# Optimization experiments

Measured on AMD Instinct MI355X. Metric: run time of the kernel, lower is better.

The kernel has to match this reference:

```python
import jax, jax.numpy as jnp
import numpy as np

B, K = 4096, 64
D_MODEL, D_DYN, D_STAT = 256, 512, 64
H = 4
DH = D_MODEL // H
SCALE = DH ** -0.5
LN_EPS = 1e-5


def _ln(x, g, b):
    m = x.mean(-1, keepdims=True)
    v = ((x - m) ** 2).mean(-1, keepdims=True)
    return (x - m) * jax.lax.rsqrt(v + LN_EPS) * g + b


def setup_inputs() -> dict:
    key = jax.random.key(0)
    ks = jax.random.split(key, 16)
    w = lambda k, s: jax.random.normal(k, s, jnp.float32) * 0.02
    return {
        "h_dyn": jax.random.normal(ks[0], (B, D_DYN), jnp.float32),
        "x_stat": jax.random.normal(ks[1], (B, K, D_STAT), jnp.float32),
        "W_dyn": w(ks[2], (D_DYN, D_MODEL)), "b_dyn": jnp.zeros((D_MODEL,)),
        "W_stat": w(ks[3], (D_STAT, D_MODEL)), "b_stat": jnp.zeros((D_MODEL,)),
        "g_ndyn": jnp.ones((D_MODEL,)), "b_ndyn": jnp.zeros((D_MODEL,)),
        "g_nstat": jnp.ones((D_MODEL,)), "b_nstat": jnp.zeros((D_MODEL,)),
        "Wq": w(ks[4], (D_MODEL, D_MODEL)), "bq": jnp.zeros((D_MODEL,)),
        "Wk": w(ks[5], (D_MODEL, D_MODEL)), "bk": jnp.zeros((D_MODEL,)),
        "Wv": w(ks[6], (D_MODEL, D_MODEL)), "bv": jnp.zeros((D_MODEL,)),
        "g_mlp": jnp.ones((D_MODEL,)), "b_mlp": jnpp if False else jnp.zeros((D_MODEL,)),
        "W1": w(ks[7], (D_MODEL, D_MODEL)), "b1": jnp.zeros((D_MODEL,)),
        "W2": w(ks[8], (D_MODEL, D_MODEL)), "b2": jnp.zeros((D_MODEL,)),
        "Wo": w(ks[9], (D_MODEL, D_MODEL)), "bo": jnp.zeros((D_MODEL,)),
        "res_scale": jnp.float32(0.1),
    }


def reference(h_dyn, x_stat, W_dyn, b_dyn, W_stat, b_stat, g_ndyn, b_ndyn,
              g_nstat, b_nstat, Wq, bq, Wk, bk, Wv, bv, g_mlp, b_mlp,
              W1, b1, W2, b2, Wo, bo, res_scale):
    h0 = h_dyn @ W_dyn + b_dyn                  # [B, d_model]
    s = x_stat @ W_stat + b_stat                # [B, K, d_model]
    h = _ln(h0, g_ndyn, b_ndyn)
    s = _ln(s, g_nstat, b_nstat)

    q = (h @ Wq + bq).reshape(B, H, DH)         # [B, H, dh]
    k = (s @ Wk + bk).reshape(B, K, H, DH)      # [B, K, H, dh]
    v_flat = s @ Wv + bv                        # [B, K, d_model]

    # per-variable MLP (DeepSets style): LN -> Linear -> GELU(exact) -> Linear
    t = _ln(v_flat, g_mlp, b_mlp)
    t = jax.nn.gelu(t @ W1 + b1, approximate=False)
    v_tokens = t @ W2 + b2                      # [B, K, d_model]

    logits = jnp.einsum('bhd,bkhd->bhk', q, k) * SCALE   # [B, H, K]
    w = jax.nn.sigmoid(logits)
    w = w / (w.sum(-1, keepdims=True) + 1e-6)

    vh = v_tokens.reshape(B, K, H, DH)
    z = jnp.einsum('bhk,bkhd->bhd', w, vh).reshape(B, D_MODEL)
    c = z @ Wo + bo
    c = h0 + res_scale * c
    w_mean = w.mean(axis=1)                     # [B, K]
    return c, w_mean
```

## Files before the change

kernel.cpp:

```cpp
#include <hip/hip_runtime.h>
#include <cmath>


typedef __bf16 bf16;
typedef bf16 bf16x4 __attribute__((ext_vector_type(4)));
typedef bf16 bf16x8 __attribute__((ext_vector_type(8)));
typedef float f32x4 __attribute__((ext_vector_type(4)));

#define MFMA_B16(a, b, c) __builtin_amdgcn_mfma_f32_16x16x32_bf16((a), (b), (c), 0, 0, 0)
#define RCP(x) __builtin_amdgcn_rcpf(x)
#define RSQ(x) __builtin_amdgcn_rsqf(x)

constexpr int SROW = 264;
constexpr int XROW = 72;

constexpr size_t WSTAT_P = 0;
constexpr size_t WV_P    = 16384;
constexpr size_t W1_P    = 81920;
constexpr size_t W2O_P   = 147456;
constexpr size_t WDYN_P  = 212992;
constexpr size_t WQ_P    = 344064;
constexpr size_t WK_P    = 409600;
constexpr size_t KQ_BF   = 475136;
constexpr size_t H0_F   = 2334720;
constexpr size_t BKQ_F  = 3383296;
constexpr size_t B2O_F  = 3399680;
constexpr size_t W2OS_F = 3399936;

__device__ __forceinline__ bf16x8 zero8() {
  bf16x8 z;
#pragma unroll
  for (int j = 0; j < 8; ++j) z[j] = (bf16)0.0f;
  return z;
}

__device__ __forceinline__ float wave_sum(float v) {
#pragma unroll
  for (int m = 1; m < 64; m <<= 1) v += __shfl_xor(v, m, 64);
  return v;
}

__device__ __forceinline__ void zero_acc(f32x4 (&acc)[4][4]) {
#pragma unroll
  for (int mt = 0; mt < 4; ++mt)
#pragma unroll
    for (int nt = 0; nt < 4; ++nt) { f32x4 z = {0.f, 0.f, 0.f, 0.f}; acc[mt][nt] = z; }
}

__device__ __forceinline__ void gemm_swapped_p(const bf16* buf, const bf16* __restrict__ Wp,
                                               int w, int lane, int l16, int koff,
                                               f32x4 (&acc)[4][4]) {
  const bf16* base = Wp + (size_t)w * 8 * 2048 + lane * 8;
  bf16x8 aw[2][4];
#pragma unroll
  for (int dt = 0; dt < 4; ++dt) aw[0][dt] = *(const bf16x8*)(base + dt * 512);
#pragma unroll
  for (int ks = 0; ks < 8; ++ks) {
    const int cur = ks & 1;
    if (ks < 7) {
#pragma unroll
      for (int dt = 0; dt < 4; ++dt)
        aw[cur ^ 1][dt] = *(const bf16x8*)(base + (ks + 1) * 2048 + dt * 512);
    }
#pragma unroll
    for (int tt = 0; tt < 4; ++tt) {
      bf16x8 bfrag = *(const bf16x8*)(buf + (tt * 16 + l16) * SROW + ks * 32 + koff);
#pragma unroll
      for (int dt = 0; dt < 4; ++dt) acc[dt][tt] = MFMA_B16(aw[cur][dt], bfrag, acc[dt][tt]);
    }
  }
}

__device__ __forceinline__ void gemm_orig_p(const bf16* buf, const bf16* __restrict__ Wp,
                                            int w, int lane, int l16, int koff,
                                            f32x4 (&acc)[4][4]) {
  const bf16* base = Wp + (size_t)w * 8 * 2048 + lane * 8;
  bf16x8 bw[2][4];
#pragma unroll
  for (int nt = 0; nt < 4; ++nt) bw[0][nt] = *(const bf16x8*)(base + nt * 512);
#pragma unroll
  for (int ks = 0; ks < 8; ++ks) {
    const int cur = ks & 1;
    if (ks < 7) {
#pragma unroll
      for (int nt = 0; nt < 4; ++nt)
        bw[cur ^ 1][nt] = *(const bf16x8*)(base + (ks + 1) * 2048 + nt * 512);
    }
#pragma unroll
    for (int mt = 0; mt < 4; ++mt) {
      bf16x8 a = *(const bf16x8*)(buf + (mt * 16 + l16) * SROW + ks * 32 + koff);
#pragma unroll
      for (int nt = 0; nt < 4; ++nt) acc[mt][nt] = MFMA_B16(a, bw[cur][nt], acc[mt][nt]);
    }
  }
}

__device__ __forceinline__ void bias_stats(f32x4 (&acc)[4][4], const float* __restrict__ bsrc,
                                           int w, int quad, int l16,
                                           float (*part_s)[64], float (*part_ss)[64]) {
  float ps[4] = {0.f, 0.f, 0.f, 0.f}, pq[4] = {0.f, 0.f, 0.f, 0.f};
#pragma unroll
  for (int dt = 0; dt < 4; ++dt) {
    const float4 bb = *(const float4*)(bsrc + w * 64 + dt * 16 + quad * 4);
#pragma unroll
    for (int tt = 0; tt < 4; ++tt) {
      float v0 = acc[dt][tt][0] + bb.x;
      float v1 = acc[dt][tt][1] + bb.y;
      float v2 = acc[dt][tt][2] + bb.z;
      float v3 = acc[dt][tt][3] + bb.w;
      acc[dt][tt][0] = v0; acc[dt][tt][1] = v1; acc[dt][tt][2] = v2; acc[dt][tt][3] = v3;
      ps[tt] += (v0 + v1) + (v2 + v3);
      pq[tt] += v0 * v0 + v1 * v1 + v2 * v2 + v3 * v3;
    }
  }
#pragma unroll
  for (int tt = 0; tt < 4; ++tt) {
    ps[tt] += __shfl_xor(ps[tt], 16, 64); ps[tt] += __shfl_xor(ps[tt], 32, 64);
    pq[tt] += __shfl_xor(pq[tt], 16, 64); pq[tt] += __shfl_xor(pq[tt], 32, 64);
  }
  if (quad == 0) {
#pragma unroll
    for (int tt = 0; tt < 4; ++tt) {
      part_s[w][tt * 16 + l16] = ps[tt];
      part_ss[w][tt * 16 + l16] = pq[tt];
    }
  }
}

__device__ __forceinline__ void ln_apply_store(f32x4 (&acc)[4][4], const float* __restrict__ g,
                                               const float* __restrict__ bsh, bf16* buf,
                                               const float (*part_s)[64],
                                               const float (*part_ss)[64],
                                               int w, int quad, int l16) {
  float mean[4], rstd[4];
#pragma unroll
  for (int tt = 0; tt < 4; ++tt) {
    const int tok = tt * 16 + l16;
    float s = (part_s[0][tok] + part_s[1][tok]) + (part_s[2][tok] + part_s[3][tok]);
    float q = (part_ss[0][tok] + part_ss[1][tok]) + (part_ss[2][tok] + part_ss[3][tok]);
    mean[tt] = s * (1.f / 256.f);
    float var = q * (1.f / 256.f) - mean[tt] * mean[tt];
    rstd[tt] = RSQ(var + 1e-5f);
  }
#pragma unroll
  for (int dt = 0; dt < 4; ++dt) {
    const float4 gv = *(const float4*)(g + w * 64 + dt * 16 + quad * 4);
    const float4 bv = *(const float4*)(bsh + w * 64 + dt * 16 + quad * 4);
#pragma unroll
    for (int tt = 0; tt < 4; ++tt) {
      float t0 = (acc[dt][tt][0] - mean[tt]) * rstd[tt];
      float t1 = (acc[dt][tt][1] - mean[tt]) * rstd[tt];
      float t2 = (acc[dt][tt][2] - mean[tt]) * rstd[tt];
      float t3 = (acc[dt][tt][3] - mean[tt]) * rstd[tt];
      bf16x4 o;
      o[0] = (bf16)(t0 * gv.x + bv.x);
      o[1] = (bf16)(t1 * gv.y + bv.y);
      o[2] = (bf16)(t2 * gv.z + bv.z);
      o[3] = (bf16)(t3 * gv.w + bv.w);
      *(bf16x4*)(buf + (tt * 16 + l16) * SROW + w * 64 + dt * 16 + quad * 4) = o;
    }
  }
}

__device__ __forceinline__ void pack_slice(const float* __restrict__ src, bf16* __restrict__ dstb,
                                           int w, int ks, bool trans, float* sh, int tid) {
  if (!trans) {
#pragma unroll
    for (int i = 0; i < 8; ++i) {
      int r = i * 4 + (tid >> 6), c = tid & 63;
      sh[r * 65 + c] = src[(size_t)(ks * 32 + r) * 256 + w * 64 + c];
    }
  } else {
    int c = tid >> 2, j8 = tid & 3;
#pragma unroll
    for (int jj = 0; jj < 8; ++jj) {
      int r = j8 * 8 + jj;
      sh[r * 65 + c] = src[(size_t)(w * 64 + c) * 256 + ks * 32 + r];
    }
  }
  __syncthreads();
  const int x = tid >> 6, quad = (tid >> 4) & 3, l16 = tid & 15;
  bf16x8 o;
#pragma unroll
  for (int j = 0; j < 8; ++j) o[j] = (bf16)sh[(quad * 8 + j) * 65 + x * 16 + l16];
  *(bf16x8*)(dstb + tid * 8) = o;
}

__global__ void prep1_kernel(const float* __restrict__ Wdyn, const float* __restrict__ Wstat,
                             const float* __restrict__ Wq, const float* __restrict__ Wk,
                             const float* __restrict__ Wv, const float* __restrict__ W1,
                             const float* __restrict__ W2, const float* __restrict__ Wo,
                             const float* __restrict__ b2,
                             bf16* __restrict__ ws, float* __restrict__ wsf) {
  __shared__ float sh[64 * 65];
  __shared__ float part[4][8];
  const int idx = blockIdx.x;
  const int tid = threadIdx.x;

  if (idx < 32) {
    const int n0 = idx * 8;
    float4 a0 = *(const float4*)(Wo + (size_t)tid * 256 + n0);
    float4 a1 = *(const float4*)(Wo + (size_t)tid * 256 + n0 + 4);
    sh[tid * 8 + 0] = a0.x; sh[tid * 8 + 1] = a0.y; sh[tid * 8 + 2] = a0.z; sh[tid * 8 + 3] = a0.w;
    sh[tid * 8 + 4] = a1.x; sh[tid * 8 + 5] = a1.y; sh[tid * 8 + 6] = a1.z; sh[tid * 8 + 7] = a1.w;
    __syncthreads();
    float acc[8] = {0.f, 0.f, 0.f, 0.f, 0.f, 0.f, 0.f, 0.f};
    const float* row = W2 + (size_t)tid * 256;
    for (int d0 = 0; d0 < 256; d0 += 4) {
      float4 wv = *(const float4*)(row + d0);
#pragma unroll
      for (int dd = 0; dd < 4; ++dd) {
        float r = (dd == 0) ? wv.x : (dd == 1) ? wv.y : (dd == 2) ? wv.z : wv.w;
        const float* cc = &sh[(d0 + dd) * 8];
#pragma unroll
        for (int j = 0; j < 8; ++j) acc[j] += r * cc[j];
      }
    }
    float* dst = wsf + W2OS_F;
#pragma unroll
    for (int j = 0; j < 8; ++j) dst[(size_t)tid * 256 + n0 + j] = acc[j];
    const int w = tid >> 6, lane = tid & 63;
    float bval = b2[tid];
#pragma unroll
    for (int j = 0; j < 8; ++j) {
      float p = wave_sum(bval * sh[tid * 8 + j]);
      if (lane == 0) part[w][j] = p;
    }
    __syncthreads();
    if (tid < 8)
      wsf[B2O_F + n0 + tid] = part[0][tid] + part[1][tid] + part[2][tid] + part[3][tid];
    return;
  }

  int t = idx - 32;
  const float* src; bf16* dst; int KS; bool trans = false;
  if (t < 64)       { src = Wdyn;  dst = ws + WDYN_P;  KS = 16; }
  else if (t < 72)  { src = Wstat; dst = ws + WSTAT_P; KS = 2;  t -= 64; }
  else if (t < 104) { src = Wq;    dst = ws + WQ_P;    KS = 8;  t -= 72; }
  else if (t < 136) { src = Wv;    dst = ws + WV_P;    KS = 8;  t -= 104; }
  else if (t < 168) { src = W1;    dst = ws + W1_P;    KS = 8;  t -= 136; }
  else              { src = Wk;    dst = ws + WK_P;    KS = 8;  t -= 168; trans = true; }
  const int w = t / KS, ks = t % KS;
  pack_slice(src, dst + (size_t)(w * KS + ks) * 2048, w, ks, trans, sh, tid);
}

__global__ void prep2_kernel(const float* __restrict__ wsf_scr, bf16* __restrict__ ws) {
  __shared__ float sh[64 * 65];
  const int t = blockIdx.x;
  pack_slice(wsf_scr, ws + W2O_P + (size_t)t * 2048, t >> 3, t & 7, false, sh, threadIdx.x);
}

__launch_bounds__(256, 2)
__global__ void pre_kernel(const float* __restrict__ h_dyn, const float* __restrict__ b_dyn,
                           const float* __restrict__ g_ndyn, const float* __restrict__ b_ndyn,
                           const float* __restrict__ bq, const float* __restrict__ bk,
                           const bf16* __restrict__ Wdyn_p, const bf16* __restrict__ Wq_p,
                           const bf16* __restrict__ Wk_p,
                           float* __restrict__ h0_out, bf16* __restrict__ kq_out,
                           float* __restrict__ bkq_out) {
  __shared__ float h0t[8][264];
  __shared__ bf16 hlnt[8][264];
  __shared__ bf16 qt[8][264];
  const int tid = threadIdx.x;
  const int w = tid >> 6, lane = tid & 63, quad = lane >> 4, l16 = lane & 15;
  const int koff = quad * 8;
  const int b0 = blockIdx.x * 8;
  const int mrow = l16 & 7;

  {
    f32x4 acc[4];
#pragma unroll
    for (int nt = 0; nt < 4; ++nt) { f32x4 z = {0.f, 0.f, 0.f, 0.f}; acc[nt] = z; }
    const float* arow = h_dyn + (size_t)(b0 + mrow) * 512;
    const bf16* base = Wdyn_p + (size_t)w * 16 * 2048 + lane * 8;
    bf16x8 bw[2][4];
#pragma unroll
    for (int nt = 0; nt < 4; ++nt) bw[0][nt] = *(const bf16x8*)(base + nt * 512);
    for (int ks = 0; ks < 16; ++ks) {
      const int cur = ks & 1;
      if (ks < 15) {
#pragma unroll
        for (int nt = 0; nt < 4; ++nt)
          bw[cur ^ 1][nt] = *(const bf16x8*)(base + (ks + 1) * 2048 + nt * 512);
      }
      float4 x0 = *(const float4*)(arow + ks * 32 + koff);
      float4 x1 = *(const float4*)(arow + ks * 32 + koff + 4);
      bf16x8 a;
      a[0] = (bf16)x0.x; a[1] = (bf16)x0.y; a[2] = (bf16)x0.z; a[3] = (bf16)x0.w;
      a[4] = (bf16)x1.x; a[5] = (bf16)x1.y; a[6] = (bf16)x1.z; a[7] = (bf16)x1.w;
#pragma unroll
      for (int nt = 0; nt < 4; ++nt) acc[nt] = MFMA_B16(a, bw[cur][nt], acc[nt]);
    }
    if (quad < 2) {
#pragma unroll
      for (int nt = 0; nt < 4; ++nt) {
        int col = w * 64 + nt * 16 + l16;
        float bb = b_dyn[col];
#pragma unroll
        for (int r = 0; r < 4; ++r) {
          int row = quad * 4 + r;
          float v = acc[nt][r] + bb;
          h0t[row][col] = v;
          h0_out[(size_t)(b0 + row) * 256 + col] = v;
        }
      }
    }
  }
  __syncthreads();

  {
    float gn[4], bn[4];
#pragma unroll
    for (int j = 0; j < 4; ++j) { gn[j] = g_ndyn[lane + 64 * j]; bn[j] = b_ndyn[lane + 64 * j]; }
#pragma unroll
    for (int i = 0; i < 2; ++i) {
      int row = 4 * i + w;
      float x[4]; float s = 0.f, ss = 0.f;
#pragma unroll
      for (int j = 0; j < 4; ++j) { x[j] = h0t[row][lane + 64 * j]; s += x[j]; ss += x[j] * x[j]; }
      s = wave_sum(s); ss = wave_sum(ss);
      float mean = s * (1.f / 256.f);
      float var = ss * (1.f / 256.f) - mean * mean;
      float rstd = RSQ(var + 1e-5f);
#pragma unroll
      for (int j = 0; j < 4; ++j)
        hlnt[row][lane + 64 * j] = (bf16)((x[j] - mean) * rstd * gn[j] + bn[j]);
    }
  }
  __syncthreads();

  {
    f32x4 acc[4];
#pragma unroll
    for (int nt = 0; nt < 4; ++nt) { f32x4 z = {0.f, 0.f, 0.f, 0.f}; acc[nt] = z; }
    const bf16* base = Wq_p + (size_t)w * 8 * 2048 + lane * 8;
    bf16x8 bw[2][4];
#pragma unroll
    for (int nt = 0; nt < 4; ++nt) bw[0][nt] = *(const bf16x8*)(base + nt * 512);
    for (int ks = 0; ks < 8; ++ks) {
      const int cur = ks & 1;
      if (ks < 7) {
#pragma unroll
        for (int nt = 0; nt < 4; ++nt)
          bw[cur ^ 1][nt] = *(const bf16x8*)(base + (ks + 1) * 2048 + nt * 512);
      }
      bf16x8 a = *(const bf16x8*)(&hlnt[mrow][ks * 32 + koff]);
#pragma unroll
      for (int nt = 0; nt < 4; ++nt) acc[nt] = MFMA_B16(a, bw[cur][nt], acc[nt]);
    }
    if (quad < 2) {
#pragma unroll
      for (int nt = 0; nt < 4; ++nt) {
        int col = w * 64 + nt * 16 + l16;
        float bb = bq[col];
#pragma unroll
        for (int r = 0; r < 4; ++r)
          qt[quad * 4 + r][col] = (bf16)(acc[nt][r] + bb);
      }
    }
  }
  __syncthreads();

  {
    const int pair = tid >> 2;
    const int row = pair >> 2, h = pair & 3, sub = tid & 3;
    if (row < 8) {
      float p = 0.f;
#pragma unroll
      for (int j = 0; j < 16; ++j) {
        int e = sub * 16 + j;
        p += (float)qt[row][h * 64 + e] * bk[h * 64 + e];
      }
      p += __shfl_xor(p, 1, 64);
      p += __shfl_xor(p, 2, 64);
      if (sub == 0) bkq_out[(size_t)(b0 + row) * 4 + h] = p;
    }
  }

  for (int h = 0; h < 4; ++h) {
    f32x4 acc[4];
#pragma unroll
    for (int nt = 0; nt < 4; ++nt) { f32x4 z = {0.f, 0.f, 0.f, 0.f}; acc[nt] = z; }
    const bf16* base = Wk_p + (size_t)w * 8 * 2048 + lane * 8;
#pragma unroll
    for (int ks = 0; ks < 2; ++ks) {
      bf16x8 a = *(const bf16x8*)(&qt[mrow][h * 64 + ks * 32 + koff]);
#pragma unroll
      for (int nt = 0; nt < 4; ++nt) {
        bf16x8 bw = *(const bf16x8*)(base + (h * 2 + ks) * 2048 + nt * 512);
        acc[nt] = MFMA_B16(a, bw, acc[nt]);
      }
    }
    if (quad < 2) {
#pragma unroll
      for (int nt = 0; nt < 4; ++nt)
#pragma unroll
        for (int r = 0; r < 4; ++r)
          kq_out[(size_t)(b0 + quad * 4 + r) * 1024 + h * 256 + w * 64 + nt * 16 + l16] =
              (bf16)acc[nt][r];
    }
  }
}

__launch_bounds__(256, 4)
__global__ void fused_kernel(
    const float* __restrict__ x_stat, const float* __restrict__ b_stat,
    const float* __restrict__ g_nstat, const float* __restrict__ b_nstat,
    const float* __restrict__ bv, const float* __restrict__ g_mlp,
    const float* __restrict__ b_mlp, const float* __restrict__ b1,
    const float* __restrict__ bo, const float* __restrict__ res_scale_p,
    const float* __restrict__ h0g, const float* __restrict__ bkq_g,
    const float* __restrict__ b2o_g,
    const bf16* __restrict__ Wstat_p, const bf16* __restrict__ Wv_p,
    const bf16* __restrict__ W1_p, const bf16* __restrict__ W2o_p,
    const bf16* __restrict__ kq_g,
    float* __restrict__ out_c, float* __restrict__ out_wm) {

  __shared__ bf16 buf[64 * SROW];
  __shared__ float part_s[4][64];
  __shared__ float part_ss[4][64];
  __shared__ float watt[4][64];
  __shared__ float swh[4];

  const int b = blockIdx.x;
  const int tid = threadIdx.x;
  const int w = tid >> 6, lane = tid & 63, quad = lane >> 4, l16 = lane & 15;
  const int koff = quad * 8;

  bf16* xs = buf;
  {
    const float* xb = x_stat + (size_t)b * 4096;
#pragma unroll
    for (int j = 0; j < 4; ++j) {
      int idx = j * 1024 + tid * 4;
      float4 v = *(const float4*)(xb + idx);
      bf16x4 o;
      o[0] = (bf16)v.x; o[1] = (bf16)v.y; o[2] = (bf16)v.z; o[3] = (bf16)v.w;
      *(bf16x4*)(xs + (idx >> 6) * XROW + (idx & 63)) = o;
    }
  }
  __syncthreads();

  {
    f32x4 acc[4][4];
    zero_acc(acc);
    const bf16* wsb = Wstat_p + (size_t)w * 2 * 2048 + lane * 8;
    bf16x8 aw[2][4];
#pragma unroll
    for (int ks = 0; ks < 2; ++ks)
#pragma unroll
      for (int dt = 0; dt < 4; ++dt)
        aw[ks][dt] = *(const bf16x8*)(wsb + ks * 2048 + dt * 512);
#pragma unroll
    for (int ks = 0; ks < 2; ++ks)
#pragma unroll
      for (int tt = 0; tt < 4; ++tt) {
        bf16x8 bfrag = *(const bf16x8*)(xs + (tt * 16 + l16) * XROW + ks * 32 + koff);
#pragma unroll
        for (int dt = 0; dt < 4; ++dt) acc[dt][tt] = MFMA_B16(aw[ks][dt], bfrag, acc[dt][tt]);
      }
    bias_stats(acc, b_stat, w, quad, l16, part_s, part_ss);
    __syncthreads();
    ln_apply_store(acc, g_nstat, b_nstat, buf, part_s, part_ss, w, quad, l16);
  }
  __syncthreads();

  {
    const bf16* kq_b = kq_g + (size_t)b * 1024;
    f32x4 accL = {0.f, 0.f, 0.f, 0.f};
#pragma unroll
    for (int ks = 0; ks < 8; ++ks) {
      bf16x8 a = *(const bf16x8*)(buf + (w * 16 + l16) * SROW + ks * 32 + koff);
      bf16x8 kf = zero8();
      if (l16 < 4) kf = *(const bf16x8*)(kq_b + l16 * 256 + ks * 32 + koff);
      accL = MFMA_B16(a, kf, accL);
    }
    float bkqv = (l16 < 4) ? bkq_g[(size_t)b * 4 + l16] : 0.f;
#pragma unroll
    for (int r = 0; r < 4; ++r) {
      float lg = (accL[r] + bkqv) * 0.125f;
      float sig = RCP(1.f + __expf(-lg));
      if (l16 < 4) watt[l16][w * 16 + quad * 4 + r] = sig;
    }
  }

  {
    f32x4 acc[4][4];
    zero_acc(acc);
    gemm_swapped_p(buf, Wv_p, w, lane, l16, koff, acc);
    bias_stats(acc, bv, w, quad, l16, part_s, part_ss);
    __syncthreads();
    {
      float v = watt[w][lane];
      float den = wave_sum(v);
      float dinv = RCP(den + 1e-6f);
      watt[w][lane] = v * dinv;
      if (lane == 0) swh[w] = den * dinv;
    }
    ln_apply_store(acc, g_mlp, b_mlp, buf, part_s, part_ss, w, quad, l16);
  }
  __syncthreads();

  if (tid < 64)
    out_wm[(size_t)b * 64 + tid] =
        0.25f * ((watt[0][tid] + watt[1][tid]) + (watt[2][tid] + watt[3][tid]));

  {
    f32x4 acc[4][4];
    zero_acc(acc);
    gemm_swapped_p(buf, W1_p, w, lane, l16, koff, acc);
    __syncthreads();
#pragma unroll
    for (int dt = 0; dt < 4; ++dt) {
      const float4 bb = *(const float4*)(b1 + w * 64 + dt * 16 + quad * 4);
#pragma unroll
      for (int tt = 0; tt < 4; ++tt) {
        float v0 = acc[dt][tt][0] + bb.x;
        float v1 = acc[dt][tt][1] + bb.y;
        float v2 = acc[dt][tt][2] + bb.z;
        float v3 = acc[dt][tt][3] + bb.w;
        bf16x4 o;
        o[0] = (bf16)(v0 * RCP(1.f + __expf(-1.702f * v0)));
        o[1] = (bf16)(v1 * RCP(1.f + __expf(-1.702f * v1)));
        o[2] = (bf16)(v2 * RCP(1.f + __expf(-1.702f * v2)));
        o[3] = (bf16)(v3 * RCP(1.f + __expf(-1.702f * v3)));
        *(bf16x4*)(buf + (tt * 16 + l16) * SROW + w * 64 + dt * 16 + quad * 4) = o;
      }
    }
  }
  __syncthreads();

  {
    f32x4 acc[4][4];
    zero_acc(acc);
    gemm_orig_p(buf, W2o_p, w, lane, l16, koff, acc);
    float zacc[4] = {0.f, 0.f, 0.f, 0.f};
#pragma unroll
    for (int mt = 0; mt < 4; ++mt)
#pragma unroll
      for (int r = 0; r < 4; ++r) {
        float wt = watt[w][mt * 16 + quad * 4 + r];
#pragma unroll
        for (int nt = 0; nt < 4; ++nt) zacc[nt] += wt * acc[mt][nt][r];
      }
#pragma unroll
    for (int nt = 0; nt < 4; ++nt) {
      zacc[nt] += __shfl_xor(zacc[nt], 16, 64);
      zacc[nt] += __shfl_xor(zacc[nt], 32, 64);
    }
    if (quad == 0) {
      float rs = *res_scale_p;
#pragma unroll
      for (int nt = 0; nt < 4; ++nt) {
        int col = w * 64 + nt * 16 + l16;
        float res = zacc[nt] + swh[w] * b2o_g[col] + bo[col];
        out_c[(size_t)b * 256 + col] = h0g[(size_t)b * 256 + col] + rs * res;
      }
    }
  }
}

extern "C" void kernel_launch(void* const* d_in, const int* in_sizes, int n_in,
                              void* d_out, int out_size, void* d_ws, size_t ws_size,
                              hipStream_t stream) {
  const float* h_dyn   = (const float*)d_in[0];
  const float* x_stat  = (const float*)d_in[1];
  const float* W_dyn   = (const float*)d_in[2];
  const float* b_dyn   = (const float*)d_in[3];
  const float* W_stat  = (const float*)d_in[4];
  const float* b_stat  = (const float*)d_in[5];
  const float* g_ndyn  = (const float*)d_in[6];
  const float* b_ndyn  = (const float*)d_in[7];
  const float* g_nstat = (const float*)d_in[8];
  const float* b_nstat = (const float*)d_in[9];
  const float* Wq = (const float*)d_in[10];
  const float* bq = (const float*)d_in[11];
  const float* Wk = (const float*)d_in[12];
  const float* bk = (const float*)d_in[13];
  const float* Wv = (const float*)d_in[14];
  const float* bv = (const float*)d_in[15];
  const float* g_mlp = (const float*)d_in[16];
  const float* b_mlp = (const float*)d_in[17];
  const float* W1 = (const float*)d_in[18];
  const float* b1 = (const float*)d_in[19];
  const float* W2 = (const float*)d_in[20];
  const float* b2 = (const float*)d_in[21];
  const float* Wo = (const float*)d_in[22];
  const float* bo = (const float*)d_in[23];
  const float* rs = (const float*)d_in[24];

  bf16* ws = (bf16*)d_ws;
  float* wsf = (float*)d_ws;

  prep1_kernel<<<232, 256, 0, stream>>>(W_dyn, W_stat, Wq, Wk, Wv, W1, W2, Wo, b2, ws, wsf);
  prep2_kernel<<<32, 256, 0, stream>>>(wsf + W2OS_F, ws);

  pre_kernel<<<512, 256, 0, stream>>>(h_dyn, b_dyn, g_ndyn, b_ndyn, bq, bk,
                                      ws + WDYN_P, ws + WQ_P, ws + WK_P,
                                      wsf + H0_F, ws + KQ_BF, wsf + BKQ_F);

  float* out_c = (float*)d_out;
  float* out_wm = out_c + (size_t)4096 * 256;
  fused_kernel<<<4096, 256, 0, stream>>>(
      x_stat, b_stat, g_nstat, b_nstat, bv, g_mlp, b_mlp, b1, bo, rs,
      wsf + H0_F, wsf + BKQ_F, wsf + B2O_F,
      ws + WSTAT_P, ws + WV_P, ws + W1_P, ws + W2O_P, ws + KQ_BF,
      out_c, out_wm);
}
```

Measured before the change: 309.3 us.

## Process two batch rows per block with 8 waves splitting output columns

The fused kernel now handles two batch elements per 512-thread block instead of one per 256-thread block. Each wave owns 32 output columns across 128 tokens, so each weight fragment loaded from global memory feeds twice as many MFMAs. This cuts weight traffic per token in exchange for doubled shared memory per block and more per-wave accumulator tiles, which may lower occupancy.

```diff
diff --git a/kernel.cpp b/kernel.cpp
--- a/kernel.cpp
+++ b/kernel.cpp
@@ -13,6 +13,7 @@
 
 constexpr int SROW = 264;
 constexpr int XROW = 72;
+constexpr int BUFE = 64 * SROW;
 
 constexpr size_t WSTAT_P = 0;
 constexpr size_t WV_P    = 16384;
@@ -40,70 +41,74 @@
   return v;
 }
 
-__device__ __forceinline__ void zero_acc(f32x4 (&acc)[4][4]) {
-#pragma unroll
-  for (int mt = 0; mt < 4; ++mt)
-#pragma unroll
-    for (int nt = 0; nt < 4; ++nt) { f32x4 z = {0.f, 0.f, 0.f, 0.f}; acc[mt][nt] = z; }
-}
-
-__device__ __forceinline__ void gemm_swapped_p(const bf16* buf, const bf16* __restrict__ Wp,
-                                               int w, int lane, int l16, int koff,
-                                               f32x4 (&acc)[4][4]) {
-  const bf16* base = Wp + (size_t)w * 8 * 2048 + lane * 8;
-  bf16x8 aw[2][4];
-#pragma unroll
-  for (int dt = 0; dt < 4; ++dt) aw[0][dt] = *(const bf16x8*)(base + dt * 512);
+__device__ __forceinline__ void zero_acc2(f32x4 (&acc)[2][8]) {
+#pragma unroll
+  for (int dt = 0; dt < 2; ++dt)
+#pragma unroll
+    for (int tt = 0; tt < 8; ++tt) { f32x4 z = {0.f, 0.f, 0.f, 0.f}; acc[dt][tt] = z; }
+}
+
+__device__ __forceinline__ void gemm_swapped_p2(const bf16* buf, const bf16* __restrict__ Wp,
+                                                int w4, int dh, int lane, int l16, int koff,
+                                                f32x4 (&acc)[2][8]) {
+  const bf16* base = Wp + (size_t)w4 * 8 * 2048 + dh * 1024 + lane * 8;
+  bf16x8 aw[2][2];
+#pragma unroll
+  for (int dt = 0; dt < 2; ++dt) aw[0][dt] = *(const bf16x8*)(base + dt * 512);
 #pragma unroll
   for (int ks = 0; ks < 8; ++ks) {
     const int cur = ks & 1;
     if (ks < 7) {
 #pragma unroll
-      for (int dt = 0; dt < 4; ++dt)
+      for (int dt = 0; dt < 2; ++dt)
         aw[cur ^ 1][dt] = *(const bf16x8*)(base + (ks + 1) * 2048 + dt * 512);
     }
 #pragma unroll
-    for (int tt = 0; tt < 4; ++tt) {
-      bf16x8 bfrag = *(const bf16x8*)(buf + (tt * 16 + l16) * SROW + ks * 32 + koff);
-#pragma unroll
-      for (int dt = 0; dt < 4; ++dt) acc[dt][tt] = MFMA_B16(aw[cur][dt], bfrag, acc[dt][tt]);
-    }
-  }
-}
-
-__device__ __forceinline__ void gemm_orig_p(const bf16* buf, const bf16* __restrict__ Wp,
-                                            int w, int lane, int l16, int koff,
-                                            f32x4 (&acc)[4][4]) {
-  const bf16* base = Wp + (size_t)w * 8 * 2048 + lane * 8;
-  bf16x8 bw[2][4];
-#pragma unroll
-  for (int nt = 0; nt < 4; ++nt) bw[0][nt] = *(const bf16x8*)(base + nt * 512);
+    for (int tt = 0; tt < 8; ++tt) {
+      bf16x8 bfrag =
+          *(const bf16x8*)(buf + (tt >> 2) * BUFE + ((tt & 3) * 16 + l16) * SROW + ks * 32 + koff);
+#pragma unroll
+      for (int dt = 0; dt < 2; ++dt) acc[dt][tt] = MFMA_B16(aw[cur][dt], bfrag, acc[dt][tt]);
+    }
+  }
+}
+
+__device__ __forceinline__ void gemm_orig_p2(const bf16* buf, const bf16* __restrict__ Wp,
+                                             int w4, int dh, int lane, int l16, int koff,
+                                             f32x4 (&acc)[2][8]) {
+  const bf16* base = Wp + (size_t)w4 * 8 * 2048 + dh * 1024 + lane * 8;
+  bf16x8 bw[2][2];
+#pragma unroll
+  for (int nt = 0; nt < 2; ++nt) bw[0][nt] = *(const bf16x8*)(base + nt * 512);
 #pragma unroll
   for (int ks = 0; ks < 8; ++ks) {
     const int cur = ks & 1;
     if (ks < 7) {
 #pragma unroll
-      for (int nt = 0; nt < 4; ++nt)
+      for (int nt = 0; nt < 2; ++nt)
         bw[cur ^ 1][nt] = *(const bf16x8*)(base + (ks + 1) * 2048 + nt * 512);
     }
 #pragma unroll
-    for (int mt = 0; mt < 4; ++mt) {
-      bf16x8 a = *(const bf16x8*)(buf + (mt * 16 + l16) * SROW + ks * 32 + koff);
-#pragma unroll
-      for (int nt = 0; nt < 4; ++nt) acc[mt][nt] = MFMA_B16(a, bw[cur][nt], acc[mt][nt]);
-    }
-  }
-}
-
-__device__ __forceinline__ void bias_stats(f32x4 (&acc)[4][4], const float* __restrict__ bsrc,
-                                           int w, int quad, int l16,
-                                           float (*part_s)[64], float (*part_ss)[64]) {
-  float ps[4] = {0.f, 0.f, 0.f, 0.f}, pq[4] = {0.f, 0.f, 0.f, 0.f};
-#pragma unroll
-  for (int dt = 0; dt < 4; ++dt) {
-    const float4 bb = *(const float4*)(bsrc + w * 64 + dt * 16 + quad * 4);
-#pragma unroll
-    for (int tt = 0; tt < 4; ++tt) {
+    for (int mt = 0; mt < 8; ++mt) {
+      bf16x8 a =
+          *(const bf16x8*)(buf + (mt >> 2) * BUFE + ((mt & 3) * 16 + l16) * SROW + ks * 32 + koff);
+#pragma unroll
+      for (int nt = 0; nt < 2; ++nt) acc[nt][mt] = MFMA_B16(a, bw[cur][nt], acc[nt][mt]);
+    }
+  }
+}
+
+__device__ __forceinline__ void bias_stats2(f32x4 (&acc)[2][8], const float* __restrict__ bsrc,
+                                            int w8, int quad, int l16,
+                                            float (*part_s)[128], float (*part_ss)[128]) {
+  float ps[8], pq[8];
+#pragma unroll
+  for (int tt = 0; tt < 8; ++tt) { ps[tt] = 0.f; pq[tt] = 0.f; }
+#pragma unroll
+  for (int dt = 0; dt < 2; ++dt) {
+    const float4 bb = *(const float4*)(bsrc + w8 * 32 + dt * 16 + quad * 4);
+#pragma unroll
+    for (int tt = 0; tt < 8; ++tt) {
       float v0 = acc[dt][tt][0] + bb.x;
       float v1 = acc[dt][tt][1] + bb.y;
       float v2 = acc[dt][tt][2] + bb.z;
@@ -114,40 +119,42 @@
     }
   }
 #pragma unroll
-  for (int tt = 0; tt < 4; ++tt) {
+  for (int tt = 0; tt < 8; ++tt) {
     ps[tt] += __shfl_xor(ps[tt], 16, 64); ps[tt] += __shfl_xor(ps[tt], 32, 64);
     pq[tt] += __shfl_xor(pq[tt], 16, 64); pq[tt] += __shfl_xor(pq[tt], 32, 64);
   }
   if (quad == 0) {
 #pragma unroll
-    for (int tt = 0; tt < 4; ++tt) {
-      part_s[w][tt * 16 + l16] = ps[tt];
-      part_ss[w][tt * 16 + l16] = pq[tt];
-    }
-  }
-}
-
-__device__ __forceinline__ void ln_apply_store(f32x4 (&acc)[4][4], const float* __restrict__ g,
-                                               const float* __restrict__ bsh, bf16* buf,
-                                               const float (*part_s)[64],
-                                               const float (*part_ss)[64],
-                                               int w, int quad, int l16) {
-  float mean[4], rstd[4];
-#pragma unroll
-  for (int tt = 0; tt < 4; ++tt) {
+    for (int tt = 0; tt < 8; ++tt) {
+      part_s[w8][tt * 16 + l16] = ps[tt];
+      part_ss[w8][tt * 16 + l16] = pq[tt];
+    }
+  }
+}
+
+__device__ __forceinline__ void ln_apply_store2(f32x4 (&acc)[2][8], const float* __restrict__ g,
+                                                const float* __restrict__ bsh, bf16* buf,
+                                                const float (*part_s)[128],
+                                                const float (*part_ss)[128],
+                                                int w8, int quad, int l16) {
+  float mean[8], rstd[8];
+#pragma unroll
+  for (int tt = 0; tt < 8; ++tt) {
     const int tok = tt * 16 + l16;
-    float s = (part_s[0][tok] + part_s[1][tok]) + (part_s[2][tok] + part_s[3][tok]);
-    float q = (part_ss[0][tok] + part_ss[1][tok]) + (part_ss[2][tok] + part_ss[3][tok]);
+    float s = ((part_s[0][tok] + part_s[1][tok]) + (part_s[2][tok] + part_s[3][tok])) +
+              ((part_s[4][tok] + part_s[5][tok]) + (part_s[6][tok] + part_s[7][tok]));
+    float q = ((part_ss[0][tok] + part_ss[1][tok]) + (part_ss[2][tok] + part_ss[3][tok])) +
+              ((part_ss[4][tok] + part_ss[5][tok]) + (part_ss[6][tok] + part_ss[7][tok]));
     mean[tt] = s * (1.f / 256.f);
     float var = q * (1.f / 256.f) - mean[tt] * mean[tt];
     rstd[tt] = RSQ(var + 1e-5f);
   }
 #pragma unroll
-  for (int dt = 0; dt < 4; ++dt) {
-    const float4 gv = *(const float4*)(g + w * 64 + dt * 16 + quad * 4);
-    const float4 bv = *(const float4*)(bsh + w * 64 + dt * 16 + quad * 4);
-#pragma unroll
-    for (int tt = 0; tt < 4; ++tt) {
+  for (int dt = 0; dt < 2; ++dt) {
+    const float4 gv = *(const float4*)(g + w8 * 32 + dt * 16 + quad * 4);
+    const float4 bv = *(const float4*)(bsh + w8 * 32 + dt * 16 + quad * 4);
+#pragma unroll
+    for (int tt = 0; tt < 8; ++tt) {
       float t0 = (acc[dt][tt][0] - mean[tt]) * rstd[tt];
       float t1 = (acc[dt][tt][1] - mean[tt]) * rstd[tt];
       float t2 = (acc[dt][tt][2] - mean[tt]) * rstd[tt];
@@ -157,7 +164,8 @@
       o[1] = (bf16)(t1 * gv.y + bv.y);
       o[2] = (bf16)(t2 * gv.z + bv.z);
       o[3] = (bf16)(t3 * gv.w + bv.w);
-      *(bf16x4*)(buf + (tt * 16 + l16) * SROW + w * 64 + dt * 16 + quad * 4) = o;
+      *(bf16x4*)(buf + (tt >> 2) * BUFE + ((tt & 3) * 16 + l16) * SROW + w8 * 32 + dt * 16 +
+                 quad * 4) = o;
     }
   }
 }
@@ -402,7 +410,7 @@
   }
 }
 
-__launch_bounds__(256, 4)
+__launch_bounds__(512, 4)
 __global__ void fused_kernel(
     const float* __restrict__ x_stat, const float* __restrict__ b_stat,
     const float* __restrict__ g_nstat, const float* __restrict__ b_nstat,
@@ -416,105 +424,111 @@
     const bf16* __restrict__ kq_g,
     float* __restrict__ out_c, float* __restrict__ out_wm) {
 
-  __shared__ bf16 buf[64 * SROW];
-  __shared__ float part_s[4][64];
-  __shared__ float part_ss[4][64];
-  __shared__ float watt[4][64];
-  __shared__ float swh[4];
-
-  const int b = blockIdx.x;
+  __shared__ bf16 buf[2 * BUFE];
+  __shared__ float part_s[8][128];
+  __shared__ float part_ss[8][128];
+  __shared__ float watt[2][4][64];
+  __shared__ float swh[2][4];
+
+  const int b0 = blockIdx.x * 2;
   const int tid = threadIdx.x;
-  const int w = tid >> 6, lane = tid & 63, quad = lane >> 4, l16 = lane & 15;
+  const int w8 = tid >> 6, lane = tid & 63, quad = lane >> 4, l16 = lane & 15;
   const int koff = quad * 8;
-
-  bf16* xs = buf;
-  {
-    const float* xb = x_stat + (size_t)b * 4096;
+  const int w4 = w8 >> 1, dh = w8 & 1;
+
+  {
+    const float* xb = x_stat + (size_t)b0 * 4096;
 #pragma unroll
     for (int j = 0; j < 4; ++j) {
-      int idx = j * 1024 + tid * 4;
+      int idx = j * 2048 + tid * 4;
       float4 v = *(const float4*)(xb + idx);
+      int bt = idx >> 12, i = idx & 4095;
       bf16x4 o;
       o[0] = (bf16)v.x; o[1] = (bf16)v.y; o[2] = (bf16)v.z; o[3] = (bf16)v.w;
-      *(bf16x4*)(xs + (idx >> 6) * XROW + (idx & 63)) = o;
-    }
-  }
-  __syncthreads();
-
-  {
-    f32x4 acc[4][4];
-    zero_acc(acc);
-    const bf16* wsb = Wstat_p + (size_t)w * 2 * 2048 + lane * 8;
-    bf16x8 aw[2][4];
+      *(bf16x4*)(buf + bt * BUFE + (i >> 6) * XROW + (i & 63)) = o;
+    }
+  }
+  __syncthreads();
+
+  {
+    f32x4 acc[2][8];
+    zero_acc2(acc);
+    const bf16* wsb = Wstat_p + (size_t)w4 * 2 * 2048 + dh * 1024 + lane * 8;
+    bf16x8 aw[2][2];
 #pragma unroll
     for (int ks = 0; ks < 2; ++ks)
 #pragma unroll
-      for (int dt = 0; dt < 4; ++dt)
+      for (int dt = 0; dt < 2; ++dt)
         aw[ks][dt] = *(const bf16x8*)(wsb + ks * 2048 + dt * 512);
 #pragma unroll
     for (int ks = 0; ks < 2; ++ks)
 #pragma unroll
-      for (int tt = 0; tt < 4; ++tt) {
-        bf16x8 bfrag = *(const bf16x8*)(xs + (tt * 16 + l16) * XROW + ks * 32 + koff);
-#pragma unroll
-        for (int dt = 0; dt < 4; ++dt) acc[dt][tt] = MFMA_B16(aw[ks][dt], bfrag, acc[dt][tt]);
-      }
-    bias_stats(acc, b_stat, w, quad, l16, part_s, part_ss);
+      for (int tt = 0; tt < 8; ++tt) {
+        bf16x8 bfrag = *(const bf16x8*)(buf + (tt >> 2) * BUFE + ((tt & 3) * 16 + l16) * XROW +
+                                        ks * 32 + koff);
+#pragma unroll
+        for (int dt = 0; dt < 2; ++dt) acc[dt][tt] = MFMA_B16(aw[ks][dt], bfrag, acc[dt][tt]);
+      }
+    bias_stats2(acc, b_stat, w8, quad, l16, part_s, part_ss);
     __syncthreads();
-    ln_apply_store(acc, g_nstat, b_nstat, buf, part_s, part_ss, w, quad, l16);
-  }
-  __syncthreads();
-
-  {
-    const bf16* kq_b = kq_g + (size_t)b * 1024;
+    ln_apply_store2(acc, g_nstat, b_nstat, buf, part_s, part_ss, w8, quad, l16);
+  }
+  __syncthreads();
+
+  {
+    const int bt = w8 >> 2, wb = w8 & 3;
+    const bf16* kq_b = kq_g + (size_t)(b0 + bt) * 1024;
     f32x4 accL = {0.f, 0.f, 0.f, 0.f};
 #pragma unroll
     for (int ks = 0; ks < 8; ++ks) {
-      bf16x8 a = *(const bf16x8*)(buf + (w * 16 + l16) * SROW + ks * 32 + koff);
+      bf16x8 a = *(const bf16x8*)(buf + bt * BUFE + (wb * 16 + l16) * SROW + ks * 32 + koff);
       bf16x8 kf = zero8();
       if (l16 < 4) kf = *(const bf16x8*)(kq_b + l16 * 256 + ks * 32 + koff);
       accL = MFMA_B16(a, kf, accL);
     }
-    float bkqv = (l16 < 4) ? bkq_g[(size_t)b * 4 + l16] : 0.f;
+    float bkqv = (l16 < 4) ? bkq_g[(size_t)(b0 + bt) * 4 + l16] : 0.f;
 #pragma unroll
     for (int r = 0; r < 4; ++r) {
       float lg = (accL[r] + bkqv) * 0.125f;
       float sig = RCP(1.f + __expf(-lg));
-      if (l16 < 4) watt[l16][w * 16 + quad * 4 + r] = sig;
-    }
-  }
-
-  {
-    f32x4 acc[4][4];
-    zero_acc(acc);
-    gemm_swapped_p(buf, Wv_p, w, lane, l16, koff, acc);
-    bias_stats(acc, bv, w, quad, l16, part_s, part_ss);
+      if (l16 < 4) watt[bt][l16][wb * 16 + quad * 4 + r] = sig;
+    }
+  }
+
+  {
+    f32x4 acc[2][8];
+    zero_acc2(acc);
+    gemm_swapped_p2(buf, Wv_p, w4, dh, lane, l16, koff, acc);
+    bias_stats2(acc, bv, w8, quad, l16, part_s, part_ss);
     __syncthreads();
     {
-      float v = watt[w][lane];
+      const int bt = w8 >> 2, h = w8 & 3;
+      float v = watt[bt][h][lane];
       float den = wave_sum(v);
       float dinv = RCP(den + 1e-6f);
-      watt[w][lane] = v * dinv;
-      if (lane == 0) swh[w] = den * dinv;
-    }
-    ln_apply_store(acc, g_mlp, b_mlp, buf, part_s, part_ss, w, quad, l16);
-  }
-  __syncthreads();
-
-  if (tid < 64)
-    out_wm[(size_t)b * 64 + tid] =
-        0.25f * ((watt[0][tid] + watt[1][tid]) + (watt[2][tid] + watt[3][tid]));
-
-  {
-    f32x4 acc[4][4];
-    zero_acc(acc);
-    gemm_swapped_p(buf, W1_p, w, lane, l16, koff, acc);
+      watt[bt][h][lane] = v * dinv;
+      if (lane == 0) swh[bt][h] = den * dinv;
+    }
+    ln_apply_store2(acc, g_mlp, b_mlp, buf, part_s, part_ss, w8, quad, l16);
+  }
+  __syncthreads();
+
+  if (tid < 128) {
+    int bt = tid >> 6, t = tid & 63;
+    out_wm[(size_t)(b0 + bt) * 64 + t] =
+        0.25f * ((watt[bt][0][t] + watt[bt][1][t]) + (watt[bt][2][t] + watt[bt][3][t]));
+  }
+
+  {
+    f32x4 acc[2][8];
+    zero_acc2(acc);
+    gemm_swapped_p2(buf, W1_p, w4, dh, lane, l16, koff, acc);
     __syncthreads();
 #pragma unroll
-    for (int dt = 0; dt < 4; ++dt) {
-      const float4 bb = *(const float4*)(b1 + w * 64 + dt * 16 + quad * 4);
-#pragma unroll
-      for (int tt = 0; tt < 4; ++tt) {
+    for (int dt = 0; dt < 2; ++dt) {
+      const float4 bb = *(const float4*)(b1 + w8 * 32 + dt * 16 + quad * 4);
+#pragma unroll
+      for (int tt = 0; tt < 8; ++tt) {
         float v0 = acc[dt][tt][0] + bb.x;
         float v1 = acc[dt][tt][1] + bb.y;
         float v2 = acc[dt][tt][2] + bb.z;
@@ -524,38 +538,47 @@
         o[1] = (bf16)(v1 * RCP(1.f + __expf(-1.702f * v1)));
         o[2] = (bf16)(v2 * RCP(1.f + __expf(-1.702f * v2)));
         o[3] = (bf16)(v3 * RCP(1.f + __expf(-1.702f * v3)));
-        *(bf16x4*)(buf + (tt * 16 + l16) * SROW + w * 64 + dt * 16 + quad * 4) = o;
-      }
-    }
-  }
-  __syncthreads();
-
-  {
-    f32x4 acc[4][4];
-    zero_acc(acc);
-    gemm_orig_p(buf, W2o_p, w, lane, l16, koff, acc);
-    float zacc[4] = {0.f, 0.f, 0.f, 0.f};
-#pragma unroll
-    for (int mt = 0; mt < 4; ++mt)
+        *(bf16x4*)(buf + (tt >> 2) * BUFE + ((tt & 3) * 16 + l16) * SROW + w8 * 32 + dt * 16 +
+                   quad * 4) = o;
+      }
+    }
+  }
+  __syncthreads();
+
+  {
+    f32x4 acc[2][8];
+    zero_acc2(acc);
+    gemm_orig_p2(buf, W2o_p, w4, dh, lane, l16, koff, acc);
+    const int h = w8 >> 1;
+    float zacc[2][2] = {{0.f, 0.f}, {0.f, 0.f}};
+#pragma unroll
+    for (int mt = 0; mt < 8; ++mt) {
+      const int bt = mt >> 2;
 #pragma unroll
       for (int r = 0; r < 4; ++r) {
-        float wt = watt[w][mt * 16 + quad * 4 + r];
-#pragma unroll
-        for (int nt = 0; nt < 4; ++nt) zacc[nt] += wt * acc[mt][nt][r];
-      }
-#pragma unroll
-    for (int nt = 0; nt < 4; ++nt) {
-      zacc[nt] += __shfl_xor(zacc[nt], 16, 64);
-      zacc[nt] += __shfl_xor(zacc[nt], 32, 64);
-    }
+        float wt = watt[bt][h][(mt & 3) * 16 + quad * 4 + r];
+#pragma unroll
+        for (int nt = 0; nt < 2; ++nt) zacc[bt][nt] += wt * acc[nt][mt][r];
+      }
+    }
+#pragma unroll
+    for (int bt = 0; bt < 2; ++bt)
+#pragma unroll
+      for (int nt = 0; nt < 2; ++nt) {
+        zacc[bt][nt] += __shfl_xor(zacc[bt][nt], 16, 64);
+        zacc[bt][nt] += __shfl_xor(zacc[bt][nt], 32, 64);
+      }
     if (quad == 0) {
       float rs = *res_scale_p;
 #pragma unroll
-      for (int nt = 0; nt < 4; ++nt) {
-        int col = w * 64 + nt * 16 + l16;
-        float res = zacc[nt] + swh[w] * b2o_g[col] + bo[col];
-        out_c[(size_t)b * 256 + col] = h0g[(size_t)b * 256 + col] + rs * res;
-      }
+      for (int bt = 0; bt < 2; ++bt)
+#pragma unroll
+        for (int nt = 0; nt < 2; ++nt) {
+          int col = w8 * 32 + nt * 16 + l16;
+          float res = zacc[bt][nt] + swh[bt][h] * b2o_g[col] + bo[col];
+          out_c[(size_t)(b0 + bt) * 256 + col] =
+              h0g[(size_t)(b0 + bt) * 256 + col] + rs * res;
+        }
     }
   }
 }
@@ -601,7 +624,7 @@
 
   float* out_c = (float*)d_out;
   float* out_wm = out_c + (size_t)4096 * 256;
-  fused_kernel<<<4096, 256, 0, stream>>>(
+  fused_kernel<<<2048, 512, 0, stream>>>(
       x_stat, b_stat, g_nstat, b_nstat, bv, g_mlp, b_mlp, b1, bo, rs,
       wsf + H0_F, wsf + BKQ_F, wsf + B2O_F,
       ws + WSTAT_P, ws + WV_P, ws + W1_P, ws + W2O_P, ws + KQ_BF,
```

Measured after the change: 351.3 us. +13.6%, slower.

## Prefetch next-stage weight fragments before barriers and fold prep2 into pre_kernel

Applied to the files above, without the earlier changes.

Loads the first k-slice of weight fragments for the next GEMM stage (Wv, W1, W2o) before the preceding __syncthreads, and hoists the Wstat fragment loads above the x_stat staging barrier. The goal is to hide global-load latency behind barrier waits. Separately, the W2/Wo packing work from prep2 is merged into pre_kernel as 32 extra blocks, which removes one kernel launch. In exchange it uses more registers for the prefetched fragments and adds a 64x65 float shared array to pre_kernel, which may lower its occupancy.

```diff
diff --git a/kernel.cpp b/kernel.cpp
--- a/kernel.cpp
+++ b/kernel.cpp
@@ -47,13 +47,21 @@
     for (int nt = 0; nt < 4; ++nt) { f32x4 z = {0.f, 0.f, 0.f, 0.f}; acc[mt][nt] = z; }
 }
 
+__device__ __forceinline__ void preload4(const bf16* __restrict__ Wp, int w, int lane,
+                                         bf16x8 (&pre)[4]) {
+  const bf16* base = Wp + (size_t)w * 8 * 2048 + lane * 8;
+#pragma unroll
+  for (int t = 0; t < 4; ++t) pre[t] = *(const bf16x8*)(base + t * 512);
+}
+
 __device__ __forceinline__ void gemm_swapped_p(const bf16* buf, const bf16* __restrict__ Wp,
                                                int w, int lane, int l16, int koff,
+                                               const bf16x8 (&pre)[4],
                                                f32x4 (&acc)[4][4]) {
   const bf16* base = Wp + (size_t)w * 8 * 2048 + lane * 8;
   bf16x8 aw[2][4];
 #pragma unroll
-  for (int dt = 0; dt < 4; ++dt) aw[0][dt] = *(const bf16x8*)(base + dt * 512);
+  for (int dt = 0; dt < 4; ++dt) aw[0][dt] = pre[dt];
 #pragma unroll
   for (int ks = 0; ks < 8; ++ks) {
     const int cur = ks & 1;
@@ -73,11 +81,12 @@
 
 __device__ __forceinline__ void gemm_orig_p(const bf16* buf, const bf16* __restrict__ Wp,
                                             int w, int lane, int l16, int koff,
+                                            const bf16x8 (&pre)[4],
                                             f32x4 (&acc)[4][4]) {
   const bf16* base = Wp + (size_t)w * 8 * 2048 + lane * 8;
   bf16x8 bw[2][4];
 #pragma unroll
-  for (int nt = 0; nt < 4; ++nt) bw[0][nt] = *(const bf16x8*)(base + nt * 512);
+  for (int nt = 0; nt < 4; ++nt) bw[0][nt] = pre[nt];
 #pragma unroll
   for (int ks = 0; ks < 8; ++ks) {
     const int cur = ks & 1;
@@ -244,24 +253,27 @@
   pack_slice(src, dst + (size_t)(w * KS + ks) * 2048, w, ks, trans, sh, tid);
 }
 
-__global__ void prep2_kernel(const float* __restrict__ wsf_scr, bf16* __restrict__ ws) {
-  __shared__ float sh[64 * 65];
-  const int t = blockIdx.x;
-  pack_slice(wsf_scr, ws + W2O_P + (size_t)t * 2048, t >> 3, t & 7, false, sh, threadIdx.x);
-}
-
 __launch_bounds__(256, 2)
 __global__ void pre_kernel(const float* __restrict__ h_dyn, const float* __restrict__ b_dyn,
                            const float* __restrict__ g_ndyn, const float* __restrict__ b_ndyn,
                            const float* __restrict__ bq, const float* __restrict__ bk,
                            const bf16* __restrict__ Wdyn_p, const bf16* __restrict__ Wq_p,
                            const bf16* __restrict__ Wk_p,
+                           const float* __restrict__ w2o_scr, bf16* __restrict__ w2o_pack,
                            float* __restrict__ h0_out, bf16* __restrict__ kq_out,
                            float* __restrict__ bkq_out) {
   __shared__ float h0t[8][264];
   __shared__ bf16 hlnt[8][264];
   __shared__ bf16 qt[8][264];
+  __shared__ float shp[64 * 65];
   const int tid = threadIdx.x;
+
+  if (blockIdx.x >= 512) {
+    const int t = blockIdx.x - 512;
+    pack_slice(w2o_scr, w2o_pack + (size_t)t * 2048, t >> 3, t & 7, false, shp, tid);
+    return;
+  }
+
   const int w = tid >> 6, lane = tid & 63, quad = lane >> 4, l16 = lane & 15;
   const int koff = quad * 8;
   const int b0 = blockIdx.x * 8;
@@ -439,30 +451,35 @@
       *(bf16x4*)(xs + (idx >> 6) * XROW + (idx & 63)) = o;
     }
   }
-  __syncthreads();
+  bf16x8 aw1[2][4];
+  {
+    const bf16* wsb = Wstat_p + (size_t)w * 2 * 2048 + lane * 8;
+#pragma unroll
+    for (int ks = 0; ks < 2; ++ks)
+#pragma unroll
+      for (int dt = 0; dt < 4; ++dt)
+        aw1[ks][dt] = *(const bf16x8*)(wsb + ks * 2048 + dt * 512);
+  }
+  __syncthreads();
+
+  bf16x8 pre[4];
 
   {
     f32x4 acc[4][4];
     zero_acc(acc);
-    const bf16* wsb = Wstat_p + (size_t)w * 2 * 2048 + lane * 8;
-    bf16x8 aw[2][4];
-#pragma unroll
-    for (int ks = 0; ks < 2; ++ks)
-#pragma unroll
-      for (int dt = 0; dt < 4; ++dt)
-        aw[ks][dt] = *(const bf16x8*)(wsb + ks * 2048 + dt * 512);
 #pragma unroll
     for (int ks = 0; ks < 2; ++ks)
 #pragma unroll
       for (int tt = 0; tt < 4; ++tt) {
         bf16x8 bfrag = *(const bf16x8*)(xs + (tt * 16 + l16) * XROW + ks * 32 + koff);
 #pragma unroll
-        for (int dt = 0; dt < 4; ++dt) acc[dt][tt] = MFMA_B16(aw[ks][dt], bfrag, acc[dt][tt]);
+        for (int dt = 0; dt < 4; ++dt) acc[dt][tt] = MFMA_B16(aw1[ks][dt], bfrag, acc[dt][tt]);
       }
     bias_stats(acc, b_stat, w, quad, l16, part_s, part_ss);
     __syncthreads();
     ln_apply_store(acc, g_nstat, b_nstat, buf, part_s, part_ss, w, quad, l16);
   }
+  preload4(Wv_p, w, lane, pre);
   __syncthreads();
 
   {
@@ -487,7 +504,7 @@
   {
     f32x4 acc[4][4];
     zero_acc(acc);
-    gemm_swapped_p(buf, Wv_p, w, lane, l16, koff, acc);
+    gemm_swapped_p(buf, Wv_p, w, lane, l16, koff, pre, acc);
     bias_stats(acc, bv, w, quad, l16, part_s, part_ss);
     __syncthreads();
     {
@@ -499,6 +516,7 @@
     }
     ln_apply_store(acc, g_mlp, b_mlp, buf, part_s, part_ss, w, quad, l16);
   }
+  preload4(W1_p, w, lane, pre);
   __syncthreads();
 
   if (tid < 64)
@@ -508,7 +526,7 @@
   {
     f32x4 acc[4][4];
     zero_acc(acc);
-    gemm_swapped_p(buf, W1_p, w, lane, l16, koff, acc);
+    gemm_swapped_p(buf, W1_p, w, lane, l16, koff, pre, acc);
     __syncthreads();
 #pragma unroll
     for (int dt = 0; dt < 4; ++dt) {
@@ -528,12 +546,13 @@
       }
     }
   }
+  preload4(W2o_p, w, lane, pre);
   __syncthreads();
 
   {
     f32x4 acc[4][4];
     zero_acc(acc);
-    gemm_orig_p(buf, W2o_p, w, lane, l16, koff, acc);
+    gemm_orig_p(buf, W2o_p, w, lane, l16, koff, pre, acc);
     float zacc[4] = {0.f, 0.f, 0.f, 0.f};
 #pragma unroll
     for (int mt = 0; mt < 4; ++mt)
@@ -593,10 +612,10 @@
   float* wsf = (float*)d_ws;
 
   prep1_kernel<<<232, 256, 0, stream>>>(W_dyn, W_stat, Wq, Wk, Wv, W1, W2, Wo, b2, ws, wsf);
-  prep2_kernel<<<32, 256, 0, stream>>>(wsf + W2OS_F, ws);
-
-  pre_kernel<<<512, 256, 0, stream>>>(h_dyn, b_dyn, g_ndyn, b_ndyn, bq, bk,
+
+  pre_kernel<<<544, 256, 0, stream>>>(h_dyn, b_dyn, g_ndyn, b_ndyn, bq, bk,
                                       ws + WDYN_P, ws + WQ_P, ws + WK_P,
+                                      wsf + W2OS_F, ws + W2O_P,
                                       wsf + H0_F, ws + KQ_BF, wsf + BKQ_F);
 
   float* out_c = (float*)d_out;
```

Result: no change. 303.6 us (-1.9%).
